# Kernel tuning notes

Measured on AMD Instinct MI355X. Metric: run time of the kernel, lower is better.

The kernel has to match this reference:

```python
import jax, jax.numpy as jnp
import numpy as np

B, N, D = 4, 2048, 1024
H = 16
d_head = D // H
N_CTX = 512


def setup_inputs() -> dict:
    key = jax.random.key(0)
    ks = jax.random.split(key, 6)
    x = jax.random.normal(ks[0], (B, N, D), dtype=jnp.float32)
    ctx_ppr = jax.random.uniform(ks[1], (N_CTX,), dtype=jnp.float32)
    ctx_trust = jax.random.normal(ks[2], (N_CTX,), dtype=jnp.float32)
    W_in = jax.random.normal(ks[3], (3 * D, D), dtype=jnp.float32) * (D ** -0.5)
    b_in = jnp.zeros((3 * D,), dtype=jnp.float32)
    W_out = jax.random.normal(ks[4], (D, D), dtype=jnp.float32) * (D ** -0.5)
    b_out = jnp.zeros((D,), dtype=jnp.float32)
    log_ppr_alpha = jnp.ones((1,), dtype=jnp.float32) * 0.1
    trust_scale = jnp.ones((1,), dtype=jnp.float32) * 0.1
    return {
        "x": x, "n_ctx": N_CTX, "ctx_ppr": ctx_ppr, "ctx_trust": ctx_trust,
        "W_in": W_in, "b_in": b_in, "W_out": W_out, "b_out": b_out,
        "log_ppr_alpha": log_ppr_alpha, "trust_scale": trust_scale,
    }


def reference(x, n_ctx, ctx_ppr, ctx_trust, W_in, b_in, W_out, b_out,
              log_ppr_alpha, trust_scale):
    Bn, Nn, Dn = x.shape
    scale = d_head ** -0.5
    # fused QKV projection: [B,N,3D]
    qkv = jnp.einsum('bnd,ed->bne', x, W_in) + b_in
    q, k, v = jnp.split(qkv, 3, axis=-1)
    # [B,H,N,d]
    def to_heads(t):
        return t.reshape(Bn, Nn, H, d_head).transpose(0, 2, 1, 3)
    q, k, v = to_heads(q), to_heads(k), to_heads(v)
    if n_ctx > 0:
        # sigmoid value gate on the first n_ctx (context) key positions
        gate = jax.nn.sigmoid(trust_scale * ctx_trust)  # [n_ctx]
        gate_full = jnp.concatenate([gate, jnp.ones((Nn - n_ctx,), x.dtype)])
        v = v * gate_full[None, None, :, None]
    logits = jnp.einsum('bhqd,bhkd->bhqk', q, k) * scale
    if n_ctx > 0:
        # additive per-key log-PPR bias on context columns
        col_bias = -log_ppr_alpha * jnp.log(jnp.clip(ctx_ppr, 1e-8))  # [n_ctx]
        col_bias_full = jnp.concatenate([col_bias, jnp.zeros((Nn - n_ctx,), x.dtype)])
        logits = logits + col_bias_full[None, None, None, :]
    weights = jax.nn.softmax(logits, axis=-1)  # dropout: eval mode (identity)
    out = jnp.einsum('bhqk,bhkd->bhqd', weights, v)
    out = out.transpose(0, 2, 1, 3).reshape(Bn, Nn, Dn)
    return jnp.einsum('bnd,ed->bne', out, W_out) + b_out
```

## Files before the change

### kernel.cpp

```cpp
#include <hip/hip_runtime.h>
#include <math.h>

typedef unsigned short u16;
typedef unsigned int   u32;
typedef __attribute__((ext_vector_type(8))) short short8;
typedef __attribute__((ext_vector_type(4))) float floatx4;

#define MFMA16(a, b, c) __builtin_amdgcn_mfma_f32_16x16x32_bf16(a, b, c, 0, 0, 0)
#define LOG2E 1.4426950408889634f

__device__ __forceinline__ float b2f(u16 b) { return __uint_as_float(((u32)b) << 16); }
__device__ __forceinline__ u16 f2b(float f) {
  u32 x = __float_as_uint(f);
  return (u16)((x + 0x7FFFu + ((x >> 16) & 1u)) >> 16);
}
__device__ __forceinline__ float fexp2(float x) {
  float r;
  asm("v_exp_f32 %0, %1" : "=v"(r) : "v"(x));
  return r;
}
__device__ __forceinline__ short8 pack8(float4 a, float4 b) {
  short8 r;
  r[0] = (short)f2b(a.x); r[1] = (short)f2b(a.y); r[2] = (short)f2b(a.z); r[3] = (short)f2b(a.w);
  r[4] = (short)f2b(b.x); r[5] = (short)f2b(b.y); r[6] = (short)f2b(b.z); r[7] = (short)f2b(b.w);
  return r;
}
__device__ __forceinline__ void gload16(const u16* g, u16* l) {
  __builtin_amdgcn_global_load_lds(
      (const __attribute__((address_space(1))) u32*)g,
      (__attribute__((address_space(3))) u32*)l, 16, 0, 0);
}
__device__ __forceinline__ int swzg(int r, int c) {
  return ((r >> 1) << 6) + (((((r & 1) << 2) | c) ^ ((r >> 1) & 7)) << 3);
}

__global__ void prep_kernel(const float* __restrict__ ppr, const float* __restrict__ trust,
                            const float* __restrict__ plpa, const float* __restrict__ ptsc,
                            const int* __restrict__ pnc,
                            float* __restrict__ colbias, float* __restrict__ vgate)
{
  const int i = blockIdx.x * 256 + threadIdx.x;
  const int n_ctx = pnc[0];
  const float lpa = plpa[0], ts = ptsc[0];
  if (i < 2048) {
    float cb = 0.0f, g = 1.0f;
    if (i < n_ctx) {
      cb = -lpa * logf(fmaxf(ppr[i], 1e-8f)) * LOG2E;
      g = 1.0f / (1.0f + expf(-ts * trust[i]));
    }
    colbias[i] = cb;
    vgate[i] = g;
  }
}

__global__ __launch_bounds__(256) void convert1(const float* __restrict__ X, const float* __restrict__ Wi,
                                                u16* __restrict__ Xb, u16* __restrict__ Wib)
{
  const size_t i = ((size_t)blockIdx.x * 256 + threadIdx.x) * 8;
  const float* src;
  u16* dst;
  if (i < 8388608) { src = X + i; dst = Xb + i; }
  else { src = Wi + (i - 8388608); dst = Wib + (i - 8388608); }
  float4 a = *(const float4*)src, b = *(const float4*)(src + 4);
  *(short8*)dst = pack8(a, b);
}

__global__ __launch_bounds__(256) void convert2(const float* __restrict__ Wo, u16* __restrict__ Wob)
{
  const size_t i = ((size_t)blockIdx.x * 256 + threadIdx.x) * 8;
  float4 a = *(const float4*)(Wo + i), b = *(const float4*)(Wo + i + 4);
  *(short8*)(Wob + i) = pack8(a, b);
}

__global__ __launch_bounds__(256, 4) void qkv_mfma(
    const u16* __restrict__ Xb, const u16* __restrict__ Wib, const float* __restrict__ bin,
    const float* __restrict__ vgate,
    u16* __restrict__ qW, u16* __restrict__ kW, u16* __restrict__ vT)
{
  __shared__ __align__(16) u16 SMEM[16384];
  const int tid = threadIdx.x;
  const int wave = tid >> 6, lane = tid & 63;
  const int k15 = lane & 15, quad = lane >> 4;
  const int wm = wave & 1, wn = wave >> 1;
  const int m0 = blockIdx.y << 7, n0 = blockIdx.x << 7;

  const int line = lane >> 3;
  const int sl = (lane & 7) ^ line;
  const int rloc = (line << 1) | (sl >> 2);
  const int cch = (sl & 3) << 3;
  const u16* gA = Xb + (size_t)(m0 + (wave << 5) + rloc) * 1024 + cch;
  const u16* gB = Wib + (size_t)(n0 + (wave << 5) + rloc) * 1024 + cch;

#define STAGE(buf, k0s) do {                                                   \
    u16* As_ = SMEM + (buf) * 8192 + (wave << 10);                             \
    gload16(gA + (k0s), As_);                                                  \
    gload16(gA + (k0s) + 16 * 1024, As_ + 512);                                \
    gload16(gB + (k0s), As_ + 4096);                                           \
    gload16(gB + (k0s) + 16 * 1024, As_ + 4608);                               \
  } while (0)

  int afo[4], bfo[4];
#pragma unroll
  for (int rt = 0; rt < 4; ++rt) afo[rt] = swzg(64 * wm + 16 * rt + k15, quad);
#pragma unroll
  for (int ct = 0; ct < 4; ++ct) bfo[ct] = 4096 + swzg(64 * wn + 16 * ct + k15, quad);

  floatx4 c[4][4];
#pragma unroll
  for (int i = 0; i < 4; ++i)
#pragma unroll
    for (int j = 0; j < 4; ++j) c[i][j] = (floatx4){0.f, 0.f, 0.f, 0.f};

  STAGE(0, 0);
  for (int k0 = 0; k0 < 1024; k0 += 32) {
    const int cur = (k0 >> 5) & 1;
    if (k0 < 992) {
      STAGE(cur ^ 1, k0 + 32);
      __builtin_amdgcn_sched_barrier(0);
      asm volatile("s_waitcnt vmcnt(4)" ::: "memory");
    } else {
      __builtin_amdgcn_sched_barrier(0);
      asm volatile("s_waitcnt vmcnt(0)" ::: "memory");
    }
    __builtin_amdgcn_sched_barrier(0);
    __builtin_amdgcn_s_barrier();
    __builtin_amdgcn_sched_barrier(0);

    const u16* Base = SMEM + cur * 8192;
    short8 af[4], bf[4];
#pragma unroll
    for (int rt = 0; rt < 4; ++rt) af[rt] = *(const short8*)(Base + afo[rt]);
#pragma unroll
    for (int ct = 0; ct < 4; ++ct) bf[ct] = *(const short8*)(Base + bfo[ct]);
    __builtin_amdgcn_s_setprio(1);
#pragma unroll
    for (int rt = 0; rt < 4; ++rt)
#pragma unroll
      for (int ct = 0; ct < 4; ++ct)
        c[rt][ct] = MFMA16(af[rt], bf[ct], c[rt][ct]);
    __builtin_amdgcn_s_setprio(0);
    __builtin_amdgcn_sched_barrier(0);
    __builtin_amdgcn_s_barrier();
    __builtin_amdgcn_sched_barrier(0);
  }
#undef STAGE

  const int which = n0 >> 10;
  if (which < 2) {
    u16* dst0 = which ? kW : qW;
    const float ksc = which ? 0.125f * LOG2E : 1.0f;
#pragma unroll
    for (int ct = 0; ct < 4; ++ct) {
      const int e = n0 + 64 * wn + 16 * ct + k15;
      const float bb = bin[e];
      const int h = (e >> 6) & 15, d = e & 63;
#pragma unroll
      for (int rt = 0; rt < 4; ++rt)
#pragma unroll
        for (int r = 0; r < 4; ++r) {
          const int m = m0 + 64 * wm + 16 * rt + 4 * quad + r;
          const int b = m >> 11, n = m & 2047;
          dst0[(((size_t)(b * 16 + h)) * 2048 + n) * 64 + d] = f2b((c[rt][ct][r] + bb) * ksc);
        }
    }
  } else {
    const int b = m0 >> 11, nbase = m0 & 2047;
    u16* T = SMEM;
    for (int half = 0; half < 2; ++half) {
      __syncthreads();
      if (wn == half) {
#pragma unroll
        for (int ct = 0; ct < 4; ++ct) {
          const int el = 16 * ct + k15;
          const int e = n0 + 64 * half + el;
          const float bb = bin[e];
#pragma unroll
          for (int rt = 0; rt < 4; ++rt)
#pragma unroll
            for (int r = 0; r < 4; ++r) {
              const int ml = 64 * wm + 16 * rt + 4 * quad + r;
              T[el * 136 + ml] = f2b((c[rt][ct][r] + bb) * vgate[nbase + ml]);
            }
        }
      }
      __syncthreads();
#pragma unroll
      for (int uu = 0; uu < 4; ++uu) {
        const int u = tid + uu * 256;
        const int el = u >> 4, moct = u & 15;
        const int e = n0 + 64 * half + el;
        const int h = (e >> 6) & 15, d = e & 63;
        short8 vv = *(const short8*)(T + el * 136 + moct * 8);
        *(short8*)(vT + (((size_t)(b * 16 + h)) * 64 + d) * 2048 + nbase + moct * 8) = vv;
      }
    }
  }
}

__global__ __launch_bounds__(256, 4) void attn_mfma(
    const u16* __restrict__ qW, const u16* __restrict__ kW, const u16* __restrict__ vT,
    const float* __restrict__ colbias, u16* __restrict__ aO)
{
  __shared__ __align__(16) u16 Kbuf[2][4096];
  __shared__ __align__(16) u16 Vbuf[2][4096];
  __shared__ __align__(16) u16 Ps[4][1024];

  const int tid = threadIdx.x;
  const int wave = tid >> 6, lane = tid & 63;
  const int k15 = lane & 15, quad = lane >> 4;
  const int bid = blockIdx.x;
  const int bh = bid & 63, qt = bid >> 6;
  const size_t base = (size_t)bh * 2048 * 64;
  const size_t baseV = (size_t)bh * 64 * 2048;
  const int q0 = qt * 128 + wave * 32;

  const int sw3 = (k15 & 7) << 3;
  const int cA = (quad * 8) ^ sw3;
  const int cB = (quad * 8 + 32) ^ sw3;

  const int krow0 = wave * 16 + (lane >> 3);
  const int swz = ((lane & 7) * 8) ^ ((lane >> 3) << 3);
  const u16* gK = kW + base + (size_t)krow0 * 64 + swz;
  const u16* gV = vT + baseV + (size_t)krow0 * 2048 + swz;

#define STAGE(nb, kbn) do {                                                    \
    gload16(gK + (size_t)(kbn) * 64, &Kbuf[nb][wave * 1024]);                  \
    gload16(gK + (size_t)(kbn) * 64 + 512, &Kbuf[nb][wave * 1024 + 512]);      \
    gload16(gV + (kbn), &Vbuf[nb][wave * 1024]);                               \
    gload16(gV + (kbn) + 8 * 2048, &Vbuf[nb][wave * 1024 + 512]);              \
  } while (0)

  const u16* qp = qW + base + (size_t)(q0 + k15) * 64 + quad * 8;
  short8 qa00 = *(const short8*)qp;
  short8 qa01 = *(const short8*)(qp + 32);
  short8 qa10 = *(const short8*)(qp + 16 * 64);
  short8 qa11 = *(const short8*)(qp + 16 * 64 + 32);

  floatx4 o0[4], o1[4];
#pragma unroll
  for (int t = 0; t < 4; ++t) {
    o0[t] = (floatx4){0.f, 0.f, 0.f, 0.f};
    o1[t] = (floatx4){0.f, 0.f, 0.f, 0.f};
  }
  floatx4 l0 = (floatx4){0.f, 0.f, 0.f, 0.f};
  floatx4 l1 = (floatx4){0.f, 0.f, 0.f, 0.f};
  float m0 = -3.0e38f, m1 = -3.0e38f;

  u16* PsW = Ps[wave];
  const short8 ones8 = (short8){16256, 16256, 16256, 16256, 16256, 16256, 16256, 16256};

  STAGE(0, 0);

  for (int kb = 0; kb < 2048; kb += 64) {
    const int cur = (kb >> 6) & 1;

    float4 cb[4];
#pragma unroll
    for (int t = 0; t < 4; ++t)
      cb[t] = *(const float4*)(colbias + kb + 16 * t + 4 * quad);
    __builtin_amdgcn_sched_barrier(0);
    if (kb < 1984) {
      STAGE(cur ^ 1, kb + 64);
      asm volatile("s_waitcnt vmcnt(4)" ::: "memory");
    } else {
      asm volatile("s_waitcnt vmcnt(0)" ::: "memory");
    }
    __builtin_amdgcn_sched_barrier(0);
    __builtin_amdgcn_s_barrier();
    __builtin_amdgcn_sched_barrier(0);

    const u16* Kc = Kbuf[cur];
    const u16* Vc = Vbuf[cur];

    floatx4 s0[4], s1[4];
    __builtin_amdgcn_s_setprio(1);
#pragma unroll
    for (int t = 0; t < 4; ++t) {
      const u16* kp = Kc + (16 * t + k15) * 64;
      short8 ka0 = *(const short8*)(kp + cA);
      short8 ka1 = *(const short8*)(kp + cB);
      floatx4 ci = (floatx4){cb[t].x, cb[t].y, cb[t].z, cb[t].w};
      s0[t] = MFMA16(ka0, qa00, ci);
      s0[t] = MFMA16(ka1, qa01, s0[t]);
      s1[t] = MFMA16(ka0, qa10, ci);
      s1[t] = MFMA16(ka1, qa11, s1[t]);
    }
    __builtin_amdgcn_s_setprio(0);

#define SOFTHALF(S, M, L, O) do {                                              \
    float mx = fmaxf(fmaxf(S[0][0], S[0][1]), fmaxf(S[0][2], S[0][3]));        \
    _Pragma("unroll") for (int t = 1; t < 4; ++t)                              \
      mx = fmaxf(mx, fmaxf(fmaxf(S[t][0], S[t][1]), fmaxf(S[t][2], S[t][3]))); \
    mx = fmaxf(mx, __shfl_xor(mx, 16));                                        \
    mx = fmaxf(mx, __shfl_xor(mx, 32));                                        \
    if (__any(mx > (M) + 8.0f)) {                                              \
      const float mn = fmaxf(M, mx);                                           \
      const float al = fexp2((M) - mn);                                        \
      M = mn;                                                                  \
      const float a0 = __shfl(al, 4 * quad + 0);                               \
      const float a1 = __shfl(al, 4 * quad + 1);                               \
      const float a2 = __shfl(al, 4 * quad + 2);                               \
      const float a3 = __shfl(al, 4 * quad + 3);                               \
      L[0] *= a0; L[1] *= a1; L[2] *= a2; L[3] *= a3;                          \
      _Pragma("unroll") for (int t = 0; t < 4; ++t) {                          \
        O[t][0] *= a0; O[t][1] *= a1; O[t][2] *= a2; O[t][3] *= a3;            \
      }                                                                        \
    }                                                                          \
    _Pragma("unroll") for (int t = 0; t < 4; ++t) {                            \
      float p0 = fexp2(S[t][0] - M), p1 = fexp2(S[t][1] - M);                  \
      float p2 = fexp2(S[t][2] - M), p3 = fexp2(S[t][3] - M);                  \
      u32 lo = __builtin_amdgcn_perm(__float_as_uint(p1), __float_as_uint(p0), 0x07060302u); \
      u32 hi = __builtin_amdgcn_perm(__float_as_uint(p3), __float_as_uint(p2), 0x07060302u); \
      *(uint2*)(PsW + k15 * 64 + ((16 * t + 4 * quad) ^ sw3)) = (uint2){lo, hi}; \
    }                                                                          \
  } while (0)

    SOFTHALF(s0, m0, l0, o0);
    short8 pa00 = *(const short8*)(PsW + k15 * 64 + cA);
    short8 pa01 = *(const short8*)(PsW + k15 * 64 + cB);
    {
      floatx4 z4 = (floatx4){0.f, 0.f, 0.f, 0.f};
      floatx4 sA = MFMA16(pa00, ones8, z4);
      sA = MFMA16(pa01, ones8, sA);
      l0 += sA;
    }
    SOFTHALF(s1, m1, l1, o1);
    short8 pa10 = *(const short8*)(PsW + k15 * 64 + cA);
    short8 pa11 = *(const short8*)(PsW + k15 * 64 + cB);
    {
      floatx4 z4 = (floatx4){0.f, 0.f, 0.f, 0.f};
      floatx4 sB = MFMA16(pa10, ones8, z4);
      sB = MFMA16(pa11, ones8, sB);
      l1 += sB;
    }

    __builtin_amdgcn_s_setprio(1);
#pragma unroll
    for (int t = 0; t < 4; ++t) {
      const u16* vp = Vc + (16 * t + k15) * 64;
      short8 vb0 = *(const short8*)(vp + cA);
      short8 vb1 = *(const short8*)(vp + cB);
      o0[t] = MFMA16(pa00, vb0, o0[t]);
      o0[t] = MFMA16(pa01, vb1, o0[t]);
      o1[t] = MFMA16(pa10, vb0, o1[t]);
      o1[t] = MFMA16(pa11, vb1, o1[t]);
    }
    __builtin_amdgcn_s_setprio(0);
    __builtin_amdgcn_sched_barrier(0);
    __builtin_amdgcn_s_barrier();
    __builtin_amdgcn_sched_barrier(0);
  }
#undef SOFTHALF
#undef STAGE

  const int b = bh >> 4, h = bh & 15;
#pragma unroll
  for (int r = 0; r < 4; ++r) {
    {
      const int q = q0 + 4 * quad + r;
      const float inv = 1.0f / l0[r];
      u16* dst = aO + (size_t)(b * 2048 + q) * 1024 + h * 64;
#pragma unroll
      for (int t = 0; t < 4; ++t) dst[16 * t + k15] = f2b(o0[t][r] * inv);
    }
    {
      const int q = q0 + 16 + 4 * quad + r;
      const float inv = 1.0f / l1[r];
      u16* dst = aO + (size_t)(b * 2048 + q) * 1024 + h * 64;
#pragma unroll
      for (int t = 0; t < 4; ++t) dst[16 * t + k15] = f2b(o1[t][r] * inv);
    }
  }
}

__global__ __launch_bounds__(256, 4) void oproj_mfma(
    const u16* __restrict__ A, const u16* __restrict__ Wob, const float* __restrict__ bout,
    float* __restrict__ out)
{
  __shared__ __align__(16) u16 SMEM[12288];
  const int tid = threadIdx.x;
  const int wave = tid >> 6, lane = tid & 63;
  const int k15 = lane & 15, quad = lane >> 4;
  const int m0 = blockIdx.y << 6, n0 = blockIdx.x << 7;

  const int line = lane >> 3;
  const int sl = (lane & 7) ^ line;
  const int rloc = (line << 1) | (sl >> 2);
  const int cch = (sl & 3) << 3;
  const u16* gA = A + (size_t)(m0 + (wave << 4) + rloc) * 1024 + cch;
  const u16* gB = Wob + (size_t)(n0 + (wave << 5) + rloc) * 1024 + cch;

#define STAGE(buf, k0s) do {                                                   \
    u16* b_ = SMEM + (buf) * 6144;                                             \
    gload16(gA + (k0s), b_ + (wave << 9));                                     \
    gload16(gB + (k0s), b_ + 2048 + (wave << 10));                             \
    gload16(gB + (k0s) + 16 * 1024, b_ + 2048 + (wave << 10) + 512);           \
  } while (0)

  int afo[4], bfo[2];
#pragma unroll
  for (int rt = 0; rt < 4; ++rt) afo[rt] = swzg(16 * rt + k15, quad);
#pragma unroll
  for (int ct = 0; ct < 2; ++ct) bfo[ct] = 2048 + swzg((wave << 5) + 16 * ct + k15, quad);

  floatx4 c[4][2];
#pragma unroll
  for (int i = 0; i < 4; ++i)
#pragma unroll
    for (int j = 0; j < 2; ++j) c[i][j] = (floatx4){0.f, 0.f, 0.f, 0.f};

  STAGE(0, 0);
  for (int k0 = 0; k0 < 1024; k0 += 32) {
    const int cur = (k0 >> 5) & 1;
    if (k0 < 992) {
      STAGE(cur ^ 1, k0 + 32);
      __builtin_amdgcn_sched_barrier(0);
      asm volatile("s_waitcnt vmcnt(3)" ::: "memory");
    } else {
      __builtin_amdgcn_sched_barrier(0);
      asm volatile("s_waitcnt vmcnt(0)" ::: "memory");
    }
    __builtin_amdgcn_sched_barrier(0);
    __builtin_amdgcn_s_barrier();
    __builtin_amdgcn_sched_barrier(0);

    const u16* Base = SMEM + cur * 6144;
    short8 af[4], bf[2];
#pragma unroll
    for (int rt = 0; rt < 4; ++rt) af[rt] = *(const short8*)(Base + afo[rt]);
#pragma unroll
    for (int ct = 0; ct < 2; ++ct) bf[ct] = *(const short8*)(Base + bfo[ct]);
    __builtin_amdgcn_s_setprio(1);
#pragma unroll
    for (int rt = 0; rt < 4; ++rt)
#pragma unroll
      for (int ct = 0; ct < 2; ++ct)
        c[rt][ct] = MFMA16(af[rt], bf[ct], c[rt][ct]);
    __builtin_amdgcn_s_setprio(0);
    __builtin_amdgcn_sched_barrier(0);
    __builtin_amdgcn_s_barrier();
    __builtin_amdgcn_sched_barrier(0);
  }
#undef STAGE

#pragma unroll
  for (int ct = 0; ct < 2; ++ct) {
    const int e = n0 + (wave << 5) + 16 * ct + k15;
    const float bb = bout[e];
#pragma unroll
    for (int rt = 0; rt < 4; ++rt)
#pragma unroll
      for (int r = 0; r < 4; ++r) {
        const int m = m0 + 16 * rt + 4 * quad + r;
        out[(size_t)m * 1024 + e] = c[rt][ct][r] + bb;
      }
  }
}

extern "C" void kernel_launch(void* const* d_in, const int* in_sizes, int n_in,
                              void* d_out, int out_size, void* d_ws, size_t ws_size,
                              hipStream_t stream)
{
  const float* X     = (const float*)d_in[0];
  const int*   pnc   = (const int*)d_in[1];
  const float* ppr   = (const float*)d_in[2];
  const float* trust = (const float*)d_in[3];
  const float* Win   = (const float*)d_in[4];
  const float* bin   = (const float*)d_in[5];
  const float* Wout  = (const float*)d_in[6];
  const float* bout  = (const float*)d_in[7];
  const float* plpa  = (const float*)d_in[8];
  const float* ptsc  = (const float*)d_in[9];
  float* out = (float*)d_out;

  const size_t SZ = (size_t)64 * 2048 * 64;
  u16* Xb = (u16*)d_ws;
  u16* qW = Xb + SZ;
  u16* kW = qW + SZ;
  u16* vT = kW + SZ;
  u16* aO = Xb;
  u16* Wob = kW;
  float* colbias = (float*)d_out;
  float* vgate   = colbias + 2048;
  u16*   Wib     = (u16*)(vgate + 2048);

  prep_kernel<<<dim3(8), 256, 0, stream>>>(ppr, trust, plpa, ptsc, pnc, colbias, vgate);
  convert1<<<dim3(5632), 256, 0, stream>>>(X, Win, Xb, Wib);
  qkv_mfma<<<dim3(24, 64), 256, 0, stream>>>(Xb, Wib, bin, vgate, qW, kW, vT);
  attn_mfma<<<dim3(1024), 256, 0, stream>>>(qW, kW, vT, colbias, aO);
  convert2<<<dim3(512), 256, 0, stream>>>(Wout, Wob);
  oproj_mfma<<<dim3(8, 128), 256, 0, stream>>>(aO, Wob, bout, out);
}
```

Before: 306.1 us.

## Drop LDS K/V staging in attention and halve per-wave query rows

The attention kernel stops staging K and V tiles through double-buffered shared memory and reads each MFMA operand straight from global memory (relying on L1/L2). Each wave now handles 16 query rows instead of 32, the grid doubles to 2048 blocks, and launch bounds target 6 blocks per CU. The aim is to remove barriers and LDS traffic and raise occupancy. In exchange, K/V reuse across waves drops, global/cache traffic per FLOP roughly doubles, and the loads are no longer prefetched ahead of use.

```diff
diff --git a/kernel.cpp b/kernel.cpp
--- a/kernel.cpp
+++ b/kernel.cpp
@@ -197,12 +197,10 @@
   }
 }
 
-__global__ __launch_bounds__(256, 4) void attn_mfma(
+__global__ __launch_bounds__(256, 6) void attn_mfma(
     const u16* __restrict__ qW, const u16* __restrict__ kW, const u16* __restrict__ vT,
     const float* __restrict__ colbias, u16* __restrict__ aO)
 {
-  __shared__ __align__(16) u16 Kbuf[2][4096];
-  __shared__ __align__(16) u16 Vbuf[2][4096];
   __shared__ __align__(16) u16 Ps[4][1024];
 
   const int tid = threadIdx.x;
@@ -212,164 +210,102 @@
   const int bh = bid & 63, qt = bid >> 6;
   const size_t base = (size_t)bh * 2048 * 64;
   const size_t baseV = (size_t)bh * 64 * 2048;
-  const int q0 = qt * 128 + wave * 32;
+  const int q0 = qt * 64 + wave * 16;
 
   const int sw3 = (k15 & 7) << 3;
   const int cA = (quad * 8) ^ sw3;
   const int cB = (quad * 8 + 32) ^ sw3;
 
-  const int krow0 = wave * 16 + (lane >> 3);
-  const int swz = ((lane & 7) * 8) ^ ((lane >> 3) << 3);
-  const u16* gK = kW + base + (size_t)krow0 * 64 + swz;
-  const u16* gV = vT + baseV + (size_t)krow0 * 2048 + swz;
-
-#define STAGE(nb, kbn) do {                                                    \
-    gload16(gK + (size_t)(kbn) * 64, &Kbuf[nb][wave * 1024]);                  \
-    gload16(gK + (size_t)(kbn) * 64 + 512, &Kbuf[nb][wave * 1024 + 512]);      \
-    gload16(gV + (kbn), &Vbuf[nb][wave * 1024]);                               \
-    gload16(gV + (kbn) + 8 * 2048, &Vbuf[nb][wave * 1024 + 512]);              \
-  } while (0)
+  const u16* gK = kW + base;
+  const u16* gV = vT + baseV;
 
   const u16* qp = qW + base + (size_t)(q0 + k15) * 64 + quad * 8;
-  short8 qa00 = *(const short8*)qp;
-  short8 qa01 = *(const short8*)(qp + 32);
-  short8 qa10 = *(const short8*)(qp + 16 * 64);
-  short8 qa11 = *(const short8*)(qp + 16 * 64 + 32);
-
-  floatx4 o0[4], o1[4];
-#pragma unroll
-  for (int t = 0; t < 4; ++t) {
-    o0[t] = (floatx4){0.f, 0.f, 0.f, 0.f};
-    o1[t] = (floatx4){0.f, 0.f, 0.f, 0.f};
-  }
-  floatx4 l0 = (floatx4){0.f, 0.f, 0.f, 0.f};
-  floatx4 l1 = (floatx4){0.f, 0.f, 0.f, 0.f};
-  float m0 = -3.0e38f, m1 = -3.0e38f;
+  short8 qa0 = *(const short8*)qp;
+  short8 qa1 = *(const short8*)(qp + 32);
+
+  floatx4 o[4];
+#pragma unroll
+  for (int t = 0; t < 4; ++t) o[t] = (floatx4){0.f, 0.f, 0.f, 0.f};
+  floatx4 l = (floatx4){0.f, 0.f, 0.f, 0.f};
+  float m = -3.0e38f;
 
   u16* PsW = Ps[wave];
   const short8 ones8 = (short8){16256, 16256, 16256, 16256, 16256, 16256, 16256, 16256};
 
-  STAGE(0, 0);
-
   for (int kb = 0; kb < 2048; kb += 64) {
-    const int cur = (kb >> 6) & 1;
-
     float4 cb[4];
 #pragma unroll
     for (int t = 0; t < 4; ++t)
       cb[t] = *(const float4*)(colbias + kb + 16 * t + 4 * quad);
-    __builtin_amdgcn_sched_barrier(0);
-    if (kb < 1984) {
-      STAGE(cur ^ 1, kb + 64);
-      asm volatile("s_waitcnt vmcnt(4)" ::: "memory");
-    } else {
-      asm volatile("s_waitcnt vmcnt(0)" ::: "memory");
-    }
-    __builtin_amdgcn_sched_barrier(0);
-    __builtin_amdgcn_s_barrier();
-    __builtin_amdgcn_sched_barrier(0);
-
-    const u16* Kc = Kbuf[cur];
-    const u16* Vc = Vbuf[cur];
-
-    floatx4 s0[4], s1[4];
+
+    floatx4 s[4];
     __builtin_amdgcn_s_setprio(1);
 #pragma unroll
     for (int t = 0; t < 4; ++t) {
-      const u16* kp = Kc + (16 * t + k15) * 64;
-      short8 ka0 = *(const short8*)(kp + cA);
-      short8 ka1 = *(const short8*)(kp + cB);
+      const u16* kp = gK + (size_t)(kb + 16 * t + k15) * 64 + quad * 8;
+      short8 ka0 = *(const short8*)kp;
+      short8 ka1 = *(const short8*)(kp + 32);
       floatx4 ci = (floatx4){cb[t].x, cb[t].y, cb[t].z, cb[t].w};
-      s0[t] = MFMA16(ka0, qa00, ci);
-      s0[t] = MFMA16(ka1, qa01, s0[t]);
-      s1[t] = MFMA16(ka0, qa10, ci);
-      s1[t] = MFMA16(ka1, qa11, s1[t]);
+      s[t] = MFMA16(ka0, qa0, ci);
+      s[t] = MFMA16(ka1, qa1, s[t]);
     }
     __builtin_amdgcn_s_setprio(0);
 
-#define SOFTHALF(S, M, L, O) do {                                              \
-    float mx = fmaxf(fmaxf(S[0][0], S[0][1]), fmaxf(S[0][2], S[0][3]));        \
-    _Pragma("unroll") for (int t = 1; t < 4; ++t)                              \
-      mx = fmaxf(mx, fmaxf(fmaxf(S[t][0], S[t][1]), fmaxf(S[t][2], S[t][3]))); \
-    mx = fmaxf(mx, __shfl_xor(mx, 16));                                        \
-    mx = fmaxf(mx, __shfl_xor(mx, 32));                                        \
-    if (__any(mx > (M) + 8.0f)) {                                              \
-      const float mn = fmaxf(M, mx);                                           \
-      const float al = fexp2((M) - mn);                                        \
-      M = mn;                                                                  \
-      const float a0 = __shfl(al, 4 * quad + 0);                               \
-      const float a1 = __shfl(al, 4 * quad + 1);                               \
-      const float a2 = __shfl(al, 4 * quad + 2);                               \
-      const float a3 = __shfl(al, 4 * quad + 3);                               \
-      L[0] *= a0; L[1] *= a1; L[2] *= a2; L[3] *= a3;                          \
-      _Pragma("unroll") for (int t = 0; t < 4; ++t) {                          \
-        O[t][0] *= a0; O[t][1] *= a1; O[t][2] *= a2; O[t][3] *= a3;            \
-      }                                                                        \
-    }                                                                          \
-    _Pragma("unroll") for (int t = 0; t < 4; ++t) {                            \
-      float p0 = fexp2(S[t][0] - M), p1 = fexp2(S[t][1] - M);                  \
-      float p2 = fexp2(S[t][2] - M), p3 = fexp2(S[t][3] - M);                  \
-      u32 lo = __builtin_amdgcn_perm(__float_as_uint(p1), __float_as_uint(p0), 0x07060302u); \
-      u32 hi = __builtin_amdgcn_perm(__float_as_uint(p3), __float_as_uint(p2), 0x07060302u); \
-      *(uint2*)(PsW + k15 * 64 + ((16 * t + 4 * quad) ^ sw3)) = (uint2){lo, hi}; \
-    }                                                                          \
-  } while (0)
-
-    SOFTHALF(s0, m0, l0, o0);
-    short8 pa00 = *(const short8*)(PsW + k15 * 64 + cA);
-    short8 pa01 = *(const short8*)(PsW + k15 * 64 + cB);
     {
-      floatx4 z4 = (floatx4){0.f, 0.f, 0.f, 0.f};
-      floatx4 sA = MFMA16(pa00, ones8, z4);
-      sA = MFMA16(pa01, ones8, sA);
-      l0 += sA;
-    }
-    SOFTHALF(s1, m1, l1, o1);
-    short8 pa10 = *(const short8*)(PsW + k15 * 64 + cA);
-    short8 pa11 = *(const short8*)(PsW + k15 * 64 + cB);
-    {
-      floatx4 z4 = (floatx4){0.f, 0.f, 0.f, 0.f};
-      floatx4 sB = MFMA16(pa10, ones8, z4);
-      sB = MFMA16(pa11, ones8, sB);
-      l1 += sB;
-    }
+      float mx = fmaxf(fmaxf(s[0][0], s[0][1]), fmaxf(s[0][2], s[0][3]));
+#pragma unroll
+      for (int t = 1; t < 4; ++t)
+        mx = fmaxf(mx, fmaxf(fmaxf(s[t][0], s[t][1]), fmaxf(s[t][2], s[t][3])));
+      mx = fmaxf(mx, __shfl_xor(mx, 16));
+      mx = fmaxf(mx, __shfl_xor(mx, 32));
+      if (__any(mx > m + 8.0f)) {
+        const float mn = fmaxf(m, mx);
+        const float al = fexp2(m - mn);
+        m = mn;
+        const float a0 = __shfl(al, 4 * quad + 0);
+        const float a1 = __shfl(al, 4 * quad + 1);
+        const float a2 = __shfl(al, 4 * quad + 2);
+        const float a3 = __shfl(al, 4 * quad + 3);
+        l[0] *= a0; l[1] *= a1; l[2] *= a2; l[3] *= a3;
+#pragma unroll
+        for (int t = 0; t < 4; ++t) {
+          o[t][0] *= a0; o[t][1] *= a1; o[t][2] *= a2; o[t][3] *= a3;
+        }
+      }
+#pragma unroll
+      for (int t = 0; t < 4; ++t) {
+        float p0 = fexp2(s[t][0] - m), p1 = fexp2(s[t][1] - m);
+        float p2 = fexp2(s[t][2] - m), p3 = fexp2(s[t][3] - m);
+        u32 lo = __builtin_amdgcn_perm(__float_as_uint(p1), __float_as_uint(p0), 0x07060302u);
+        u32 hi = __builtin_amdgcn_perm(__float_as_uint(p3), __float_as_uint(p2), 0x07060302u);
+        *(uint2*)(PsW + k15 * 64 + ((16 * t + 4 * quad) ^ sw3)) = (uint2){lo, hi};
+      }
+    }
+
+    short8 pa0 = *(const short8*)(PsW + k15 * 64 + cA);
+    short8 pa1 = *(const short8*)(PsW + k15 * 64 + cB);
+    l = MFMA16(pa1, ones8, MFMA16(pa0, ones8, l));
 
     __builtin_amdgcn_s_setprio(1);
 #pragma unroll
     for (int t = 0; t < 4; ++t) {
-      const u16* vp = Vc + (16 * t + k15) * 64;
-      short8 vb0 = *(const short8*)(vp + cA);
-      short8 vb1 = *(const short8*)(vp + cB);
-      o0[t] = MFMA16(pa00, vb0, o0[t]);
-      o0[t] = MFMA16(pa01, vb1, o0[t]);
-      o1[t] = MFMA16(pa10, vb0, o1[t]);
-      o1[t] = MFMA16(pa11, vb1, o1[t]);
+      const u16* vp = gV + (size_t)(16 * t + k15) * 2048 + kb + quad * 8;
+      short8 vb0 = *(const short8*)vp;
+      short8 vb1 = *(const short8*)(vp + 32);
+      o[t] = MFMA16(pa0, vb0, o[t]);
+      o[t] = MFMA16(pa1, vb1, o[t]);
     }
     __builtin_amdgcn_s_setprio(0);
-    __builtin_amdgcn_sched_barrier(0);
-    __builtin_amdgcn_s_barrier();
-    __builtin_amdgcn_sched_barrier(0);
-  }
-#undef SOFTHALF
-#undef STAGE
+  }
 
   const int b = bh >> 4, h = bh & 15;
 #pragma unroll
   for (int r = 0; r < 4; ++r) {
-    {
-      const int q = q0 + 4 * quad + r;
-      const float inv = 1.0f / l0[r];
-      u16* dst = aO + (size_t)(b * 2048 + q) * 1024 + h * 64;
-#pragma unroll
-      for (int t = 0; t < 4; ++t) dst[16 * t + k15] = f2b(o0[t][r] * inv);
-    }
-    {
-      const int q = q0 + 16 + 4 * quad + r;
-      const float inv = 1.0f / l1[r];
-      u16* dst = aO + (size_t)(b * 2048 + q) * 1024 + h * 64;
-#pragma unroll
-      for (int t = 0; t < 4; ++t) dst[16 * t + k15] = f2b(o1[t][r] * inv);
-    }
+    const int q = q0 + 4 * quad + r;
+    const float inv = 1.0f / l[r];
+    u16* dst = aO + (size_t)(b * 2048 + q) * 1024 + h * 64;
+#pragma unroll
+    for (int t = 0; t < 4; ++t) dst[16 * t + k15] = f2b(o[t][r] * inv);
   }
 }
 
@@ -487,7 +423,7 @@
   prep_kernel<<<dim3(8), 256, 0, stream>>>(ppr, trust, plpa, ptsc, pnc, colbias, vgate);
   convert1<<<dim3(5632), 256, 0, stream>>>(X, Win, Xb, Wib);
   qkv_mfma<<<dim3(24, 64), 256, 0, stream>>>(Xb, Wib, bin, vgate, qW, kW, vT);
-  attn_mfma<<<dim3(1024), 256, 0, stream>>>(qW, kW, vT, colbias, aO);
+  attn_mfma<<<dim3(2048), 256, 0, stream>>>(qW, kW, vT, colbias, aO);
   convert2<<<dim3(512), 256, 0, stream>>>(Wout, Wob);
   oproj_mfma<<<dim3(8, 128), 256, 0, stream>>>(aO, Wob, bout, out);
 }
```

New measurement: 733.7 us. 140% more time.
